# Kernel tuning notes

Measured on AMD Instinct MI355X. Metric: run time of the kernel, lower is better.

The kernel has to match this reference:

```python
import jax, jax.numpy as jnp
import numpy as np

COMMITMENT_COST = 0.25

def setup_inputs() -> dict:
    key = jax.random.key(0)
    k1, k2 = jax.random.split(key)
    z = jax.random.normal(k1, (8, 2048, 768), dtype=jnp.float32)
    # codebook initialized uniform(-1/K, 1/K) in the original; use same scale
    K = 2048
    emb = jax.random.uniform(k2, (K, 768), dtype=jnp.float32, minval=-1.0 / K, maxval=1.0 / K)
    return {"z": z, "emb": emb}

def reference(z, emb):
    B, S, D = z.shape
    z_flat = z.reshape(-1, D)                                   # [N, D]
    # squared-euclidean distances via expansion: ||z||^2 + ||e||^2 - 2 z e^T
    distances = (
        jnp.sum(z_flat * z_flat, axis=1, keepdims=True)
        + jnp.sum(emb * emb, axis=1)
        - 2.0 * jnp.matmul(z_flat, emb.T)
    )                                                           # [N, K]
    ids_flat = jnp.argmin(distances, axis=1)                    # [N]
    z_q = emb[ids_flat].reshape(z.shape)                        # gather + reshape
    concept_ids = ids_flat.reshape(B, S)
    # training path with use_ema=True: codebook_loss = 0, commitment term only.
    # NOTE: original (faithfully) computes mse(z.detach(), z_q) — grad flows to z_q.
    commitment_loss = jnp.mean((jax.lax.stop_gradient(z) - z_q) ** 2)
    vq_loss = COMMITMENT_COST * commitment_loss
    # straight-through estimator
    z_q_st = z + jax.lax.stop_gradient(z_q - z)
    return z_q_st, concept_ids, vq_loss
```

## Files before the change

### kernel.cpp

```cpp
#include <hip/hip_runtime.h>
#include <float.h>

typedef unsigned short ushort_t;
typedef unsigned int uint_t;

#define NROWS 16384
#define DDIM  768
#define KCODES 2048
#define NCB2   8
#define MARGIN 8e-4f

__device__ __forceinline__ ushort_t f2bf(float x) {
    uint_t u = __float_as_uint(x);
    uint_t r = (u + 0x7fffu + ((u >> 16) & 1u)) >> 16;
    return (ushort_t)r;
}
__device__ __forceinline__ float bf2f(ushort_t h) {
    return __uint_as_float(((uint_t)h) << 16);
}

__global__ void prep_kernel(const float* __restrict__ z, const float* __restrict__ emb,
                            float* __restrict__ ee, float* __restrict__ zz,
                            ushort_t* __restrict__ Zh, ushort_t* __restrict__ Eh,
                            float* __restrict__ out_loss) {
    const int b = blockIdx.x, t = threadIdx.x;
    if (b == 0 && t == 0) out_loss[0] = 0.f;
    if (b < KCODES) {
        const int c = b;
        const float* e = emb + (size_t)c * DDIM;
        float s = 0.f;
        for (int i = t; i < DDIM; i += 256) { float v = e[i]; s += v * v; }
        for (int off = 32; off; off >>= 1) s += __shfl_down(s, off);
        __shared__ float red[4];
        if ((t & 63) == 0) red[t >> 6] = s;
        __syncthreads();
        if (t == 0) ee[c] = red[0] + red[1] + red[2] + red[3];
        if (t < 192) {
            const float4 v = ((const float4*)e)[t];
            ushort4 h;
            h.x = f2bf(v.x); h.y = f2bf(v.y); h.z = f2bf(v.z); h.w = f2bf(v.w);
            ((ushort4*)(Eh + (size_t)c * DDIM))[t] = h;
        }
    } else {
        const int rb = b - KCODES;
        const int row = rb * 4 + (t >> 6);
        const int lane = t & 63;
        const float* zr = z + (size_t)row * DDIM;
        float s = 0.f;
        for (int i = lane; i < DDIM; i += 64) { float v = zr[i]; s += v * v; }
        for (int off = 32; off; off >>= 1) s += __shfl_down(s, off);
        if (lane == 0) zz[row] = s;
        const float4* zr4 = (const float4*)zr;
        ushort4* dh = (ushort4*)(Zh + (size_t)row * DDIM);
        #pragma unroll
        for (int j = 0; j < 3; ++j) {
            const int i4 = lane + 64 * j;
            const float4 v = zr4[i4];
            ushort4 h;
            h.x = f2bf(v.x); h.y = f2bf(v.y); h.z = f2bf(v.z); h.w = f2bf(v.w);
            dh[i4] = h;
        }
    }
}

typedef __attribute__((ext_vector_type(8))) short bf16x8;
typedef __attribute__((ext_vector_type(4))) float f32x4;

__device__ __forceinline__ int swz(int r) { return (r & 3) ^ ((r >> 2) & 3); }

__global__ __launch_bounds__(256, 2)
void mfma_kernel(const ushort_t* __restrict__ Ab, const ushort_t* __restrict__ Bb,
                 const float* __restrict__ ee, float* __restrict__ bmin,
                 float2* __restrict__ slots) {
    __shared__ __align__(16) char smem[24576];
    float* rowmin = (float*)smem;
    int*   rcnt   = (int*)(smem + 512);
    float (*sval)[8] = (float(*)[8])(smem + 1024);
    int   (*sidx)[8] = (int(*)[8])(smem + 5120);

    const int t = threadIdx.x;
    const int w = t >> 6, l = t & 63;
    const int bx = blockIdx.x & 127;
    const int by = blockIdx.x >> 7;
    const int row0 = bx << 7;
    const int col0 = by << 8;

    f32x4 acc[4][8];
    #pragma unroll
    for (int i = 0; i < 4; ++i)
        #pragma unroll
        for (int j = 0; j < 8; ++j) acc[i][j] = (f32x4){0.f, 0.f, 0.f, 0.f};

    const int sri = l >> 2, slot = l & 3;
    const ushort_t* gA[2]; uint_t lA[2];
    #pragma unroll
    for (int q = 0; q < 2; ++q) {
        const int r0 = ((w << 1) + q) << 4;
        const int ra = r0 + sri;
        const int c  = slot ^ swz(ra);
        gA[q] = Ab + (size_t)(row0 + ra) * DDIM + (c << 3);
        lA[q] = r0 << 6;
    }
    const ushort_t* gB[4]; uint_t lB[4];
    #pragma unroll
    for (int q = 0; q < 4; ++q) {
        const int r0 = ((w << 2) + q) << 4;
        const int ra = r0 + sri;
        const int c  = slot ^ swz(ra);
        gB[q] = Bb + (size_t)(col0 + ra) * DDIM + (c << 3);
        lB[q] = 8192 + (r0 << 6);
    }

    const int rha = (w & 1) << 6;
    const int chb = (w >> 1) << 7;
    const ushort_t* aAddr[4]; const ushort_t* bAddr[8];
    #pragma unroll
    for (int mi = 0; mi < 4; ++mi) {
        const int r = rha + (mi << 4) + (l & 15);
        const int sw = (l >> 4) ^ swz(r);
        aAddr[mi] = (const ushort_t*)(smem + (r << 6) + (sw << 4));
    }
    #pragma unroll
    for (int ni = 0; ni < 8; ++ni) {
        const int r = chb + (ni << 4) + (l & 15);
        const int sw = (l >> 4) ^ swz(r);
        bAddr[ni] = (const ushort_t*)(smem + 8192 + (r << 6) + (sw << 4));
    }

    for (int kt = 0; kt < 24; ++kt) {
        __syncthreads();
        #pragma unroll
        for (int q = 0; q < 2; ++q) {
            __builtin_amdgcn_global_load_lds(
                (const __attribute__((address_space(1))) void*)gA[q],
                (__attribute__((address_space(3))) void*)(smem + lA[q]), 16, 0, 0);
            gA[q] += 32;
        }
        #pragma unroll
        for (int q = 0; q < 4; ++q) {
            __builtin_amdgcn_global_load_lds(
                (const __attribute__((address_space(1))) void*)gB[q],
                (__attribute__((address_space(3))) void*)(smem + lB[q]), 16, 0, 0);
            gB[q] += 32;
        }
        __syncthreads();

        bf16x8 af[4], bfr[8];
        #pragma unroll
        for (int mi = 0; mi < 4; ++mi) af[mi] = *(const bf16x8*)aAddr[mi];
        #pragma unroll
        for (int ni = 0; ni < 8; ++ni) bfr[ni] = *(const bf16x8*)bAddr[ni];
        #pragma unroll
        for (int mi = 0; mi < 4; ++mi)
            #pragma unroll
            for (int ni = 0; ni < 8; ++ni)
                acc[mi][ni] = __builtin_amdgcn_mfma_f32_16x16x32_bf16(
                    af[mi], bfr[ni], acc[mi][ni], 0, 0, 0);
    }

    __syncthreads();

    float ecv[8];
    #pragma unroll
    for (int ni = 0; ni < 8; ++ni) ecv[ni] = ee[col0 + chb + (ni << 4) + (l & 15)];
    #pragma unroll
    for (int mi = 0; mi < 4; ++mi)
        #pragma unroll
        for (int ni = 0; ni < 8; ++ni)
            #pragma unroll
            for (int r = 0; r < 4; ++r)
                acc[mi][ni][r] = ecv[ni] - 2.0f * acc[mi][ni][r];

    float vmr[4][4];
    #pragma unroll
    for (int mi = 0; mi < 4; ++mi)
        #pragma unroll
        for (int r = 0; r < 4; ++r) {
            float v = acc[mi][0][r];
            #pragma unroll
            for (int ni = 1; ni < 8; ++ni) v = fminf(v, acc[mi][ni][r]);
            v = fminf(v, __shfl_xor(v, 1));
            v = fminf(v, __shfl_xor(v, 2));
            v = fminf(v, __shfl_xor(v, 4));
            v = fminf(v, __shfl_xor(v, 8));
            vmr[mi][r] = v;
        }

    if (t < 128) { rowmin[t] = FLT_MAX; rcnt[t] = 0; }
    __syncthreads();
    if (w < 2 && (l & 15) == 0) {
        #pragma unroll
        for (int mi = 0; mi < 4; ++mi)
            #pragma unroll
            for (int r = 0; r < 4; ++r)
                rowmin[rha + (mi << 4) + ((l >> 4) << 2) + r] = vmr[mi][r];
    }
    __syncthreads();
    if (w >= 2 && (l & 15) == 0) {
        #pragma unroll
        for (int mi = 0; mi < 4; ++mi)
            #pragma unroll
            for (int r = 0; r < 4; ++r) {
                const int m = rha + (mi << 4) + ((l >> 4) << 2) + r;
                rowmin[m] = fminf(rowmin[m], vmr[mi][r]);
            }
    }
    __syncthreads();

    #pragma unroll
    for (int mi = 0; mi < 4; ++mi)
        #pragma unroll
        for (int r = 0; r < 4; ++r) {
            const int m = rha + (mi << 4) + ((l >> 4) << 2) + r;
            const float lim = rowmin[m] + MARGIN;
            #pragma unroll
            for (int ni = 0; ni < 8; ++ni) {
                const float vv = acc[mi][ni][r];
                if (vv <= lim) {
                    const int p = atomicAdd(&rcnt[m], 1);
                    if (p < 8) {
                        sval[m][p] = vv;
                        sidx[m][p] = col0 + chb + (ni << 4) + (l & 15);
                    }
                }
            }
        }
    __syncthreads();

    if (t < 128) {
        const int row = row0 + t;
        bmin[(size_t)by * NROWS + row] = rowmin[t];
        const int n = rcnt[t] < 8 ? rcnt[t] : 8;
        float2 rec[8];
        #pragma unroll
        for (int s2 = 0; s2 < 8; ++s2)
            rec[s2] = (s2 < n) ? make_float2(sval[t][s2], __int_as_float(sidx[t][s2]))
                               : make_float2(FLT_MAX, __int_as_float(0x7fffffff));
        float4* dst = (float4*)(slots + ((size_t)by * NROWS + row) * 8);
        dst[0] = make_float4(rec[0].x, rec[0].y, rec[1].x, rec[1].y);
        dst[1] = make_float4(rec[2].x, rec[2].y, rec[3].x, rec[3].y);
        dst[2] = make_float4(rec[4].x, rec[4].y, rec[5].x, rec[5].y);
        dst[3] = make_float4(rec[6].x, rec[6].y, rec[7].x, rec[7].y);
    }
}

__global__ __launch_bounds__(256)
void combine_select_gather(const float* __restrict__ bmin, const float2* __restrict__ slots,
                           const float* __restrict__ ee, const float* __restrict__ zz,
                           const float* __restrict__ z, const float* __restrict__ emb,
                           float* __restrict__ ids_f32, float* __restrict__ out0,
                           float* __restrict__ out_loss) {
    const int t = threadIdx.x;
    const int w = t >> 6;
    const int row = blockIdx.x * 4 + w;
    const int l = t & 63;

    float v = (l < NCB2) ? bmin[(size_t)l * NROWS + row] : FLT_MAX;
    v = fminf(v, __shfl_xor(v, 4));
    v = fminf(v, __shfl_xor(v, 2));
    v = fminf(v, __shfl_xor(v, 1));
    const float T = __shfl(v, 0) + MARGIN;

    const int blk = l >> 3;
    const int s0 = l & 7;
    const float2 a = slots[((size_t)blk * NROWS + row) * 8 + s0];

    unsigned long long m = __ballot(a.x <= T);

    const float zzr = zz[row];
    const float* zr = z + (size_t)row * DDIM;

    float bestd = FLT_MAX; int besti = 0x7fffffff;
    while (m) {
        const int j = __ffsll(m) - 1; m &= m - 1;
        const int idx = __float_as_int(__shfl(a.y, j));
        const float* er = emb + (size_t)idx * DDIM;
        float p = 0.f;
        #pragma unroll
        for (int k = 0; k < 12; ++k) p += zr[l + 64 * k] * er[l + 64 * k];
        for (int off = 32; off; off >>= 1) p += __shfl_down(p, off);
        if (l == 0) {
            const float t1 = zzr + ee[idx];
            const float d  = t1 - 2.0f * p;
            if (d < bestd || (d == bestd && idx < besti)) { bestd = d; besti = idx; }
        }
    }
    const int bi = __shfl(besti, 0);
    if (l == 0) ids_f32[row] = (float)bi;

    const float4* zr4 = (const float4*)zr;
    const float4* er4 = (const float4*)(emb + (size_t)bi * DDIM);
    float4* o4 = (float4*)(out0 + (size_t)row * DDIM);
    float s = 0.f;
    #pragma unroll
    for (int j = 0; j < 3; ++j) {
        const int i4 = l + 64 * j;
        const float4 zv = zr4[i4];
        const float4 ev = er4[i4];
        float4 o;
        o.x = zv.x + (ev.x - zv.x); o.y = zv.y + (ev.y - zv.y);
        o.z = zv.z + (ev.z - zv.z); o.w = zv.w + (ev.w - zv.w);
        o4[i4] = o;
        const float dx = zv.x - ev.x, dy = zv.y - ev.y;
        const float dz = zv.z - ev.z, dw = zv.w - ev.w;
        s += dx * dx + dy * dy + dz * dz + dw * dw;
    }
    for (int off = 32; off; off >>= 1) s += __shfl_down(s, off);
    __shared__ float lred[4];
    if (l == 0) lred[w] = s;
    __syncthreads();
    if (t == 0) {
        const float tot = lred[0] + lred[1] + lred[2] + lred[3];
        atomicAdd(out_loss, tot * (0.25f / (float)((size_t)NROWS * DDIM)));
    }
}

__global__ void ee_kernel(const float* __restrict__ emb, float* __restrict__ ee) {
    int c = blockIdx.x;
    const float* e = emb + (size_t)c * DDIM;
    int t = threadIdx.x;
    float s = 0.f;
    for (int i = t; i < DDIM; i += 256) { float v = e[i]; s += v * v; }
    for (int off = 32; off; off >>= 1) s += __shfl_down(s, off);
    __shared__ float red[4];
    if ((t & 63) == 0) red[t >> 6] = s;
    __syncthreads();
    if (t == 0) ee[c] = red[0] + red[1] + red[2] + red[3];
}

__global__ void zz_kernel(const float* __restrict__ z, float* __restrict__ zz) {
    const int t = threadIdx.x;
    const int row = blockIdx.x * 4 + (t >> 6);
    const int lane = t & 63;
    const float* zr = z + (size_t)row * DDIM;
    float s = 0.f;
    for (int i = lane; i < DDIM; i += 64) { float v = zr[i]; s += v * v; }
    for (int off = 32; off; off >>= 1) s += __shfl_down(s, off);
    if (lane == 0) zz[row] = s;
}

#define BM 32
#define BN 128
#define BKS 32
#define SPLITC 2
#define CODES_PER_BLOCK (KCODES / SPLITC)
#define NCHUNK (CODES_PER_BLOCK / BN)
#define NSTAGE (DDIM / BKS)
#define APADR 33
#define BPADC 132

__global__ __launch_bounds__(256)
void argmin_kernel(const float* __restrict__ z, const float* __restrict__ emb,
                   const float* __restrict__ ee, const float* __restrict__ zz,
                   float* __restrict__ pval, int* __restrict__ pidx) {
    __shared__ float Af[BKS][APADR];
    __shared__ float Bf[BKS][BPADC];
    __shared__ float cval[BM][33];
    __shared__ int   cidx[BM][33];
    __shared__ float zzs[BM];
    const int t = threadIdx.x;
    const int part = blockIdx.x & (SPLITC - 1);
    const int rb = blockIdx.x >> 1;
    const int row0 = rb * BM;
    const int cbase = part * CODES_PER_BLOCK;
    const int tx = t & 31, ty = t >> 5;
    const int sr = t >> 3;
    const int sk = 4 * (t & 7);
    if (t < BM) zzs[t] = zz[row0 + t];
    float bv[4]; int bi[4];
    #pragma unroll
    for (int i = 0; i < 4; ++i) { bv[i] = FLT_MAX; bi[i] = 0x7fffffff; }
    const float* zt = z + (size_t)(row0 + sr) * DDIM;
    for (int chunk = 0; chunk < NCHUNK; ++chunk) {
        const int c0 = cbase + chunk * BN;
        const float* ebase = emb + (size_t)(c0 + sr) * DDIM;
        float acc[4][4];
        #pragma unroll
        for (int i = 0; i < 4; ++i)
            #pragma unroll
            for (int j = 0; j < 4; ++j) acc[i][j] = 0.f;
        float4 pa = *(const float4*)&zt[sk];
        float4 pb[4];
        #pragma unroll
        for (int m = 0; m < 4; ++m) pb[m] = *(const float4*)&ebase[(size_t)(32 * m) * DDIM + sk];
        for (int s = 0; s < NSTAGE; ++s) {
            __syncthreads();
            Af[sk + 0][sr] = pa.x; Af[sk + 1][sr] = pa.y;
            Af[sk + 2][sr] = pa.z; Af[sk + 3][sr] = pa.w;
            #pragma unroll
            for (int m = 0; m < 4; ++m) {
                Bf[sk + 0][sr + 32 * m] = pb[m].x;
                Bf[sk + 1][sr + 32 * m] = pb[m].y;
                Bf[sk + 2][sr + 32 * m] = pb[m].z;
                Bf[sk + 3][sr + 32 * m] = pb[m].w;
            }
            __syncthreads();
            if (s + 1 < NSTAGE) {
                const int k1 = (s + 1) * BKS + sk;
                pa = *(const float4*)&zt[k1];
                #pragma unroll
                for (int m = 0; m < 4; ++m)
                    pb[m] = *(const float4*)&ebase[(size_t)(32 * m) * DDIM + k1];
            }
            #pragma unroll
            for (int kk = 0; kk < BKS; ++kk) {
                const float4 a4 = *(const float4*)&Af[kk][4 * ty];
                const float4 b4 = *(const float4*)&Bf[kk][4 * tx];
                const float aa[4] = {a4.x, a4.y, a4.z, a4.w};
                const float bb[4] = {b4.x, b4.y, b4.z, b4.w};
                #pragma unroll
                for (int i = 0; i < 4; ++i)
                    #pragma unroll
                    for (int j = 0; j < 4; ++j) acc[i][j] += aa[i] * bb[j];
            }
        }
        const float4 e4 = *(const float4*)&ee[c0 + 4 * tx];
        const float eev[4] = {e4.x, e4.y, e4.z, e4.w};
        #pragma unroll
        for (int i = 0; i < 4; ++i) {
            const float zzr = zzs[4 * ty + i];
            #pragma unroll
            for (int j = 0; j < 4; ++j) {
                const int code = c0 + 4 * tx + j;
                const float t1 = zzr + eev[j];
                const float d  = t1 - 2.0f * acc[i][j];
                if (d < bv[i] || (d == bv[i] && code < bi[i])) { bv[i] = d; bi[i] = code; }
            }
        }
    }
    __syncthreads();
    #pragma unroll
    for (int i = 0; i < 4; ++i) { cval[4 * ty + i][tx] = bv[i]; cidx[4 * ty + i][tx] = bi[i]; }
    __syncthreads();
    if (t < BM) {
        float v = FLT_MAX; int id = 0x7fffffff;
        #pragma unroll
        for (int x = 0; x < 32; ++x) {
            const float cv = cval[t][x]; const int ci = cidx[t][x];
            if (cv < v || (cv == v && ci < id)) { v = cv; id = ci; }
        }
        pval[part * NROWS + row0 + t] = v;
        pidx[part * NROWS + row0 + t] = id;
    }
}

__global__ void combine_kernel(const float* __restrict__ pval, const int* __restrict__ pidx,
                               float* __restrict__ ids_f32) {
    const int r = blockIdx.x * 256 + threadIdx.x;
    float v = pval[r];           int id = pidx[r];
    const float v1 = pval[NROWS + r]; const int i1 = pidx[NROWS + r];
    if (v1 < v || (v1 == v && i1 < id)) { v = v1; id = i1; }
    ids_f32[r] = (float)id;
}

__global__ __launch_bounds__(256)
void gather_kernel(const float* __restrict__ z, const float* __restrict__ emb,
                   const float* __restrict__ ids_f32, float* __restrict__ out0,
                   float* __restrict__ part) {
    const int b = blockIdx.x;
    const int t = threadIdx.x;
    const int rl = t >> 4, c = t & 15;
    __shared__ int ids[16];
    if (t < 16) ids[t] = (int)ids_f32[b * 16 + t];
    __syncthreads();
    const int row = b * 16 + rl;
    const float4* zr = (const float4*)(z + (size_t)row * DDIM);
    float4* orow = (float4*)(out0 + (size_t)row * DDIM);
    const float4* er = (const float4*)(emb + (size_t)ids[rl] * DDIM);
    float s = 0.f;
    #pragma unroll
    for (int j = 0; j < 12; ++j) {
        const int i4 = c + 16 * j;
        const float4 zv = zr[i4];
        const float4 ev = er[i4];
        float4 o;
        o.x = zv.x + (ev.x - zv.x); o.y = zv.y + (ev.y - zv.y);
        o.z = zv.z + (ev.z - zv.z); o.w = zv.w + (ev.w - zv.w);
        orow[i4] = o;
        float dx = zv.x - ev.x, dy = zv.y - ev.y, dz = zv.z - ev.z, dw = zv.w - ev.w;
        s += dx * dx + dy * dy + dz * dz + dw * dw;
    }
    for (int off = 32; off; off >>= 1) s += __shfl_down(s, off);
    __shared__ float red[4];
    if ((t & 63) == 0) red[t >> 6] = s;
    __syncthreads();
    if (t == 0) part[b] = red[0] + red[1] + red[2] + red[3];
}

__global__ void loss_kernel(const float* __restrict__ part, float* __restrict__ out_loss) {
    const int t = threadIdx.x;
    double s = 0.0;
    for (int i = t; i < 1024; i += 256) s += (double)part[i];
    for (int off = 32; off; off >>= 1) s += __shfl_down(s, off);
    __shared__ double red[4];
    if ((t & 63) == 0) red[t >> 6] = s;
    __syncthreads();
    if (t == 0) {
        const double total = red[0] + red[1] + red[2] + red[3];
        out_loss[0] = (float)(0.25 * (total / (double)((size_t)NROWS * DDIM)));
    }
}

#define EE_OFF   0
#define ZZ_OFF   8192
#define EH_OFF   73728
#define ZH_OFF   (EH_OFF + (size_t)KCODES * DDIM * 2)
#define BMIN_OFF (ZH_OFF + (size_t)NROWS * DDIM * 2)
#define SLOT_OFF (BMIN_OFF + (size_t)NCB2 * NROWS * 4)
#define WS_NEED  (SLOT_OFF + (size_t)NCB2 * NROWS * 8 * 8)
#define PART_OFF 73728
#define PV_OFF   81920

extern "C" void kernel_launch(void* const* d_in, const int* in_sizes, int n_in,
                              void* d_out, int out_size, void* d_ws, size_t ws_size,
                              hipStream_t stream) {
    const float* z   = (const float*)d_in[0];
    const float* emb = (const float*)d_in[1];

    float* out0     = (float*)d_out;
    float* out_ids  = out0 + (size_t)NROWS * DDIM;
    float* out_loss = out_ids + NROWS;

    char* ws = (char*)d_ws;
    float* ee   = (float*)(ws + EE_OFF);
    float* zzws = (float*)(ws + ZZ_OFF);

    if (ws_size >= WS_NEED) {
        ushort_t* Eh   = (ushort_t*)(ws + EH_OFF);
        ushort_t* Zh   = (ushort_t*)(ws + ZH_OFF);
        float*    bmin = (float*)(ws + BMIN_OFF);
        float2*   slot = (float2*)(ws + SLOT_OFF);
        prep_kernel<<<KCODES + NROWS / 4, 256, 0, stream>>>(z, emb, ee, zzws, Zh, Eh, out_loss);
        mfma_kernel<<<(NROWS / 128) * NCB2, 256, 0, stream>>>(Zh, Eh, ee, bmin, slot);
        combine_select_gather<<<NROWS / 4, 256, 0, stream>>>(bmin, slot, ee, zzws, z, emb,
                                                             out_ids, out0, out_loss);
    } else {
        float* part = (float*)(ws + PART_OFF);
        float* pval = (float*)(ws + PV_OFF);
        int*   pidx = (int*)(ws + PV_OFF + 131072);
        ee_kernel<<<KCODES, 256, 0, stream>>>(emb, ee);
        zz_kernel<<<NROWS / 4, 256, 0, stream>>>(z, zzws);
        argmin_kernel<<<(NROWS / BM) * SPLITC, 256, 0, stream>>>(z, emb, ee, zzws, pval, pidx);
        combine_kernel<<<NROWS / 256, 256, 0, stream>>>(pval, pidx, out_ids);
        gather_kernel<<<NROWS / 16, 256, 0, stream>>>(z, emb, out_ids, out0, part);
        loss_kernel<<<1, 256, 0, stream>>>(part, out_loss);
    }
}
```

Measured before the change: 241.4 us.

## Fuse bf16 conversion, MFMA distance argmin, refinement and gather into one kernel

The z-to-bf16 conversion, the row-norm computation, the MFMA distance search over all codes, candidate refinement, gather and loss are merged into a single kernel. Each 512-thread block keeps its 64 rows of z in LDS and streams the bf16 codebook through a double-buffered LDS tile in chunks of 128 codes. A running per-row minimum is kept with encoded-float atomicMin, and near-minimum candidates are collected per chunk. This removes the Zh, bmin and slot workspace round trips and two launches. In exchange, each block re-reads the whole codebook, uses small 2x2 MFMA tiles per wave, synchronises every k-step, and the large LDS footprint likely allows only one block per CU.

```diff
diff --git a/kernel.cpp b/kernel.cpp
--- a/kernel.cpp
+++ b/kernel.cpp
@@ -7,7 +7,6 @@
 #define NROWS 16384
 #define DDIM  768
 #define KCODES 2048
-#define NCB2   8
 #define MARGIN 8e-4f
 
 __device__ __forceinline__ ushort_t f2bf(float x) {
@@ -15,302 +14,283 @@
     uint_t r = (u + 0x7fffu + ((u >> 16) & 1u)) >> 16;
     return (ushort_t)r;
 }
-__device__ __forceinline__ float bf2f(ushort_t h) {
-    return __uint_as_float(((uint_t)h) << 16);
-}
-
-__global__ void prep_kernel(const float* __restrict__ z, const float* __restrict__ emb,
-                            float* __restrict__ ee, float* __restrict__ zz,
-                            ushort_t* __restrict__ Zh, ushort_t* __restrict__ Eh,
-                            float* __restrict__ out_loss) {
-    const int b = blockIdx.x, t = threadIdx.x;
-    if (b == 0 && t == 0) out_loss[0] = 0.f;
-    if (b < KCODES) {
-        const int c = b;
-        const float* e = emb + (size_t)c * DDIM;
-        float s = 0.f;
-        for (int i = t; i < DDIM; i += 256) { float v = e[i]; s += v * v; }
-        for (int off = 32; off; off >>= 1) s += __shfl_down(s, off);
-        __shared__ float red[4];
-        if ((t & 63) == 0) red[t >> 6] = s;
-        __syncthreads();
-        if (t == 0) ee[c] = red[0] + red[1] + red[2] + red[3];
-        if (t < 192) {
-            const float4 v = ((const float4*)e)[t];
-            ushort4 h;
-            h.x = f2bf(v.x); h.y = f2bf(v.y); h.z = f2bf(v.z); h.w = f2bf(v.w);
-            ((ushort4*)(Eh + (size_t)c * DDIM))[t] = h;
-        }
-    } else {
-        const int rb = b - KCODES;
-        const int row = rb * 4 + (t >> 6);
-        const int lane = t & 63;
+
+__device__ __forceinline__ uint_t fenc(float f) {
+    uint_t u = __float_as_uint(f);
+    return (u & 0x80000000u) ? ~u : (u | 0x80000000u);
+}
+__device__ __forceinline__ float fdec(uint_t k) {
+    uint_t u = (k & 0x80000000u) ? (k ^ 0x80000000u) : ~k;
+    return __uint_as_float(u);
+}
+
+typedef __attribute__((ext_vector_type(8))) short bf16x8;
+typedef __attribute__((ext_vector_type(4))) float f32x4;
+
+__global__ void prep2_kernel(const float* __restrict__ emb, float* __restrict__ ee,
+                             ushort_t* __restrict__ Eh, float* __restrict__ out_loss) {
+    const int c = blockIdx.x, t = threadIdx.x;
+    if (c == 0 && t == 0) out_loss[0] = 0.f;
+    const float* e = emb + (size_t)c * DDIM;
+    float s = 0.f;
+    for (int i = t; i < DDIM; i += 256) { float v = e[i]; s += v * v; }
+    for (int off = 32; off; off >>= 1) s += __shfl_down(s, off);
+    __shared__ float red[4];
+    if ((t & 63) == 0) red[t >> 6] = s;
+    __syncthreads();
+    if (t == 0) ee[c] = red[0] + red[1] + red[2] + red[3];
+    if (t < 192) {
+        const float4 v = ((const float4*)e)[t];
+        ushort4 h;
+        h.x = f2bf(v.x); h.y = f2bf(v.y); h.z = f2bf(v.z); h.w = f2bf(v.w);
+        ((ushort4*)(Eh + (size_t)c * DDIM))[t] = h;
+    }
+}
+
+#define WGROWS   64
+#define CHUNK    128
+#define NCHUNKS  16
+#define KSTEPS   12
+#define CAP      16
+#define B_OFF    98304
+#define RMIN_OFF 131072
+#define RCNT_OFF 131328
+#define SVAL_OFF 131584
+#define SIDX_OFF 135680
+#define LRED_OFF 139776
+#define SMEM_BYTES 139808
+
+__global__ __launch_bounds__(512, 2)
+void fused_kernel(const float* __restrict__ z, const float* __restrict__ emb,
+                  const ushort_t* __restrict__ Eh, const float* __restrict__ ee,
+                  float* __restrict__ ids_f32, float* __restrict__ out0,
+                  float* __restrict__ out_loss) {
+    __shared__ __align__(16) char smem[SMEM_BYTES];
+    uint_t* rowminU = (uint_t*)(smem + RMIN_OFF);
+    int*    rcnt    = (int*)(smem + RCNT_OFF);
+    float (*sval)[CAP] = (float(*)[CAP])(smem + SVAL_OFF);
+    int   (*sidx)[CAP] = (int(*)[CAP])(smem + SIDX_OFF);
+    float*  lred    = (float*)(smem + LRED_OFF);
+
+    const int t = threadIdx.x;
+    const int w = t >> 6, l = t & 63;
+    const int row0 = blockIdx.x * WGROWS;
+
+    if (t < 64) { rowminU[t] = 0xFFFFFFFFu; rcnt[t] = 0; }
+
+    float zzr[8];
+    #pragma unroll
+    for (int rr = 0; rr < 8; ++rr) {
+        const int row = row0 + w * 8 + rr;
         const float* zr = z + (size_t)row * DDIM;
         float s = 0.f;
-        for (int i = lane; i < DDIM; i += 64) { float v = zr[i]; s += v * v; }
+        #pragma unroll
+        for (int k = 0; k < 12; ++k) { const float v = zr[l + 64 * k]; s += v * v; }
         for (int off = 32; off; off >>= 1) s += __shfl_down(s, off);
-        if (lane == 0) zz[row] = s;
-        const float4* zr4 = (const float4*)zr;
-        ushort4* dh = (ushort4*)(Zh + (size_t)row * DDIM);
-        #pragma unroll
-        for (int j = 0; j < 3; ++j) {
-            const int i4 = lane + 64 * j;
-            const float4 v = zr4[i4];
-            ushort4 h;
-            h.x = f2bf(v.x); h.y = f2bf(v.y); h.z = f2bf(v.z); h.w = f2bf(v.w);
-            dh[i4] = h;
-        }
-    }
-}
-
-typedef __attribute__((ext_vector_type(8))) short bf16x8;
-typedef __attribute__((ext_vector_type(4))) float f32x4;
-
-__device__ __forceinline__ int swz(int r) { return (r & 3) ^ ((r >> 2) & 3); }
-
-__global__ __launch_bounds__(256, 2)
-void mfma_kernel(const ushort_t* __restrict__ Ab, const ushort_t* __restrict__ Bb,
-                 const float* __restrict__ ee, float* __restrict__ bmin,
-                 float2* __restrict__ slots) {
-    __shared__ __align__(16) char smem[24576];
-    float* rowmin = (float*)smem;
-    int*   rcnt   = (int*)(smem + 512);
-    float (*sval)[8] = (float(*)[8])(smem + 1024);
-    int   (*sidx)[8] = (int(*)[8])(smem + 5120);
-
-    const int t = threadIdx.x;
-    const int w = t >> 6, l = t & 63;
-    const int bx = blockIdx.x & 127;
-    const int by = blockIdx.x >> 7;
-    const int row0 = bx << 7;
-    const int col0 = by << 8;
-
-    f32x4 acc[4][8];
-    #pragma unroll
-    for (int i = 0; i < 4; ++i)
-        #pragma unroll
-        for (int j = 0; j < 8; ++j) acc[i][j] = (f32x4){0.f, 0.f, 0.f, 0.f};
-
-    const int sri = l >> 2, slot = l & 3;
-    const ushort_t* gA[2]; uint_t lA[2];
+        zzr[rr] = __shfl(s, 0);
+    }
+
+    {
+        const int ar = t >> 3;
+        const int as = t & 7;
+        const float4* zr4 = (const float4*)(z + (size_t)(row0 + ar) * DDIM);
+        char* abase = smem + ar * 1536;
+        const int rx = (ar & 7) << 4;
+        #pragma unroll
+        for (int j = 0; j < 12; ++j) {
+            const int slot = as + 8 * j;
+            const float4 v0 = zr4[2 * slot];
+            const float4 v1 = zr4[2 * slot + 1];
+            ushort4 h0, h1;
+            h0.x = f2bf(v0.x); h0.y = f2bf(v0.y); h0.z = f2bf(v0.z); h0.w = f2bf(v0.w);
+            h1.x = f2bf(v1.x); h1.y = f2bf(v1.y); h1.z = f2bf(v1.z); h1.w = f2bf(v1.w);
+            char* p = abase + ((slot << 4) ^ rx);
+            *(ushort4*)p = h0;
+            *(ushort4*)(p + 8) = h1;
+        }
+    }
+
+    const int brow_l  = l >> 3;
+    const int srcslot = (l & 7) ^ brow_l;
+    const ushort_t* gB[2];
     #pragma unroll
     for (int q = 0; q < 2; ++q) {
-        const int r0 = ((w << 1) + q) << 4;
-        const int ra = r0 + sri;
-        const int c  = slot ^ swz(ra);
-        gA[q] = Ab + (size_t)(row0 + ra) * DDIM + (c << 3);
-        lA[q] = r0 << 6;
-    }
-    const ushort_t* gB[4]; uint_t lB[4];
-    #pragma unroll
-    for (int q = 0; q < 4; ++q) {
-        const int r0 = ((w << 2) + q) << 4;
-        const int ra = r0 + sri;
-        const int c  = slot ^ swz(ra);
-        gB[q] = Bb + (size_t)(col0 + ra) * DDIM + (c << 3);
-        lB[q] = 8192 + (r0 << 6);
-    }
-
-    const int rha = (w & 1) << 6;
-    const int chb = (w >> 1) << 7;
-    const ushort_t* aAddr[4]; const ushort_t* bAddr[8];
-    #pragma unroll
-    for (int mi = 0; mi < 4; ++mi) {
-        const int r = rha + (mi << 4) + (l & 15);
-        const int sw = (l >> 4) ^ swz(r);
-        aAddr[mi] = (const ushort_t*)(smem + (r << 6) + (sw << 4));
-    }
-    #pragma unroll
-    for (int ni = 0; ni < 8; ++ni) {
-        const int r = chb + (ni << 4) + (l & 15);
-        const int sw = (l >> 4) ^ swz(r);
-        bAddr[ni] = (const ushort_t*)(smem + 8192 + (r << 6) + (sw << 4));
-    }
-
-    for (int kt = 0; kt < 24; ++kt) {
+        const int grow = q * 64 + w * 8 + brow_l;
+        gB[q] = Eh + (size_t)grow * DDIM + srcslot * 8;
+    }
+
+    const int wr = w >> 2, wc = w & 3;
+    const int g = l >> 4, lr = l & 15;
+    int aoff[2][2], boff[2][2];
+    #pragma unroll
+    for (int mi = 0; mi < 2; ++mi) {
+        const int arow = wr * 32 + mi * 16 + lr;
+        #pragma unroll
+        for (int kf = 0; kf < 2; ++kf)
+            aoff[mi][kf] = arow * 1536 + ((((kf << 2) + g) << 4) ^ ((arow & 7) << 4));
+    }
+    #pragma unroll
+    for (int ni = 0; ni < 2; ++ni) {
+        const int brow = wc * 32 + ni * 16 + lr;
+        #pragma unroll
+        for (int kf = 0; kf < 2; ++kf)
+            boff[ni][kf] = brow * 128 + ((((kf << 2) + g) << 4) ^ ((brow & 7) << 4));
+    }
+
+    int cur = 0;
+    #pragma unroll
+    for (int q = 0; q < 2; ++q) {
+        __builtin_amdgcn_global_load_lds(
+            (const __attribute__((address_space(1))) void*)gB[q],
+            (__attribute__((address_space(3))) void*)(smem + B_OFF + q * 8192 + w * 1024),
+            16, 0, 0);
+        gB[q] += 64;
+    }
+    __syncthreads();
+
+    for (int c = 0; c < NCHUNKS; ++c) {
+        const int c0 = c * CHUNK;
+        f32x4 acc[2][2];
+        #pragma unroll
+        for (int mi = 0; mi < 2; ++mi)
+            #pragma unroll
+            for (int ni = 0; ni < 2; ++ni) acc[mi][ni] = (f32x4){0.f, 0.f, 0.f, 0.f};
+
+        for (int s = 0; s < KSTEPS; ++s) {
+            if (!(c == NCHUNKS - 1 && s == KSTEPS - 1)) {
+                const int nb = B_OFF + (cur ^ 1) * 16384 + w * 1024;
+                #pragma unroll
+                for (int q = 0; q < 2; ++q)
+                    __builtin_amdgcn_global_load_lds(
+                        (const __attribute__((address_space(1))) void*)gB[q],
+                        (__attribute__((address_space(3))) void*)(smem + nb + q * 8192),
+                        16, 0, 0);
+                const int adv = (s == KSTEPS - 2) ? (64 + 127 * 768) : 64;
+                gB[0] += adv; gB[1] += adv;
+            }
+            const char* Bb = smem + B_OFF + cur * 16384;
+            bf16x8 af[2][2], bfv[2][2];
+            #pragma unroll
+            for (int mi = 0; mi < 2; ++mi)
+                #pragma unroll
+                for (int kf = 0; kf < 2; ++kf)
+                    af[mi][kf] = *(const bf16x8*)(smem + aoff[mi][kf] + s * 128);
+            #pragma unroll
+            for (int ni = 0; ni < 2; ++ni)
+                #pragma unroll
+                for (int kf = 0; kf < 2; ++kf)
+                    bfv[ni][kf] = *(const bf16x8*)(Bb + boff[ni][kf]);
+            #pragma unroll
+            for (int kf = 0; kf < 2; ++kf)
+                #pragma unroll
+                for (int mi = 0; mi < 2; ++mi)
+                    #pragma unroll
+                    for (int ni = 0; ni < 2; ++ni)
+                        acc[mi][ni] = __builtin_amdgcn_mfma_f32_16x16x32_bf16(
+                            af[mi][kf], bfv[ni][kf], acc[mi][ni], 0, 0, 0);
+            __syncthreads();
+            cur ^= 1;
+        }
+
+        float ecv[2];
+        #pragma unroll
+        for (int ni = 0; ni < 2; ++ni) ecv[ni] = ee[c0 + wc * 32 + ni * 16 + lr];
+        float dv[2][2][4];
+        #pragma unroll
+        for (int mi = 0; mi < 2; ++mi)
+            #pragma unroll
+            for (int ni = 0; ni < 2; ++ni)
+                #pragma unroll
+                for (int r = 0; r < 4; ++r)
+                    dv[mi][ni][r] = ecv[ni] - 2.0f * acc[mi][ni][r];
+
+        #pragma unroll
+        for (int mi = 0; mi < 2; ++mi)
+            #pragma unroll
+            for (int r = 0; r < 4; ++r) {
+                float v = fminf(dv[mi][0][r], dv[mi][1][r]);
+                v = fminf(v, __shfl_xor(v, 1));
+                v = fminf(v, __shfl_xor(v, 2));
+                v = fminf(v, __shfl_xor(v, 4));
+                v = fminf(v, __shfl_xor(v, 8));
+                if (lr == 0) atomicMin(&rowminU[wr * 32 + mi * 16 + g * 4 + r], fenc(v));
+            }
         __syncthreads();
         #pragma unroll
-        for (int q = 0; q < 2; ++q) {
-            __builtin_amdgcn_global_load_lds(
-                (const __attribute__((address_space(1))) void*)gA[q],
-                (__attribute__((address_space(3))) void*)(smem + lA[q]), 16, 0, 0);
-            gA[q] += 32;
-        }
-        #pragma unroll
-        for (int q = 0; q < 4; ++q) {
-            __builtin_amdgcn_global_load_lds(
-                (const __attribute__((address_space(1))) void*)gB[q],
-                (__attribute__((address_space(3))) void*)(smem + lB[q]), 16, 0, 0);
-            gB[q] += 32;
-        }
-        __syncthreads();
-
-        bf16x8 af[4], bfr[8];
-        #pragma unroll
-        for (int mi = 0; mi < 4; ++mi) af[mi] = *(const bf16x8*)aAddr[mi];
-        #pragma unroll
-        for (int ni = 0; ni < 8; ++ni) bfr[ni] = *(const bf16x8*)bAddr[ni];
-        #pragma unroll
-        for (int mi = 0; mi < 4; ++mi)
-            #pragma unroll
-            for (int ni = 0; ni < 8; ++ni)
-                acc[mi][ni] = __builtin_amdgcn_mfma_f32_16x16x32_bf16(
-                    af[mi], bfr[ni], acc[mi][ni], 0, 0, 0);
-    }
-
-    __syncthreads();
-
-    float ecv[8];
-    #pragma unroll
-    for (int ni = 0; ni < 8; ++ni) ecv[ni] = ee[col0 + chb + (ni << 4) + (l & 15)];
-    #pragma unroll
-    for (int mi = 0; mi < 4; ++mi)
-        #pragma unroll
-        for (int ni = 0; ni < 8; ++ni)
-            #pragma unroll
-            for (int r = 0; r < 4; ++r)
-                acc[mi][ni][r] = ecv[ni] - 2.0f * acc[mi][ni][r];
-
-    float vmr[4][4];
-    #pragma unroll
-    for (int mi = 0; mi < 4; ++mi)
-        #pragma unroll
-        for (int r = 0; r < 4; ++r) {
-            float v = acc[mi][0][r];
-            #pragma unroll
-            for (int ni = 1; ni < 8; ++ni) v = fminf(v, acc[mi][ni][r]);
-            v = fminf(v, __shfl_xor(v, 1));
-            v = fminf(v, __shfl_xor(v, 2));
-            v = fminf(v, __shfl_xor(v, 4));
-            v = fminf(v, __shfl_xor(v, 8));
-            vmr[mi][r] = v;
-        }
-
-    if (t < 128) { rowmin[t] = FLT_MAX; rcnt[t] = 0; }
-    __syncthreads();
-    if (w < 2 && (l & 15) == 0) {
-        #pragma unroll
-        for (int mi = 0; mi < 4; ++mi)
-            #pragma unroll
-            for (int r = 0; r < 4; ++r)
-                rowmin[rha + (mi << 4) + ((l >> 4) << 2) + r] = vmr[mi][r];
-    }
-    __syncthreads();
-    if (w >= 2 && (l & 15) == 0) {
-        #pragma unroll
-        for (int mi = 0; mi < 4; ++mi)
+        for (int mi = 0; mi < 2; ++mi)
             #pragma unroll
             for (int r = 0; r < 4; ++r) {
-                const int m = rha + (mi << 4) + ((l >> 4) << 2) + r;
-                rowmin[m] = fminf(rowmin[m], vmr[mi][r]);
-            }
-    }
-    __syncthreads();
-
-    #pragma unroll
-    for (int mi = 0; mi < 4; ++mi)
-        #pragma unroll
-        for (int r = 0; r < 4; ++r) {
-            const int m = rha + (mi << 4) + ((l >> 4) << 2) + r;
-            const float lim = rowmin[m] + MARGIN;
-            #pragma unroll
-            for (int ni = 0; ni < 8; ++ni) {
-                const float vv = acc[mi][ni][r];
-                if (vv <= lim) {
-                    const int p = atomicAdd(&rcnt[m], 1);
-                    if (p < 8) {
-                        sval[m][p] = vv;
-                        sidx[m][p] = col0 + chb + (ni << 4) + (l & 15);
+                const int lrow = wr * 32 + mi * 16 + g * 4 + r;
+                const float lim = fdec(rowminU[lrow]) + MARGIN;
+                #pragma unroll
+                for (int ni = 0; ni < 2; ++ni) {
+                    const float vv = dv[mi][ni][r];
+                    if (vv <= lim) {
+                        const int p = atomicAdd(&rcnt[lrow], 1);
+                        if (p < CAP) {
+                            sval[lrow][p] = vv;
+                            sidx[lrow][p] = c0 + wc * 32 + ni * 16 + lr;
+                        }
                     }
                 }
             }
-        }
-    __syncthreads();
-
-    if (t < 128) {
-        const int row = row0 + t;
-        bmin[(size_t)by * NROWS + row] = rowmin[t];
-        const int n = rcnt[t] < 8 ? rcnt[t] : 8;
-        float2 rec[8];
-        #pragma unroll
-        for (int s2 = 0; s2 < 8; ++s2)
-            rec[s2] = (s2 < n) ? make_float2(sval[t][s2], __int_as_float(sidx[t][s2]))
-                               : make_float2(FLT_MAX, __int_as_float(0x7fffffff));
-        float4* dst = (float4*)(slots + ((size_t)by * NROWS + row) * 8);
-        dst[0] = make_float4(rec[0].x, rec[0].y, rec[1].x, rec[1].y);
-        dst[1] = make_float4(rec[2].x, rec[2].y, rec[3].x, rec[3].y);
-        dst[2] = make_float4(rec[4].x, rec[4].y, rec[5].x, rec[5].y);
-        dst[3] = make_float4(rec[6].x, rec[6].y, rec[7].x, rec[7].y);
-    }
-}
-
-__global__ __launch_bounds__(256)
-void combine_select_gather(const float* __restrict__ bmin, const float2* __restrict__ slots,
-                           const float* __restrict__ ee, const float* __restrict__ zz,
-                           const float* __restrict__ z, const float* __restrict__ emb,
-                           float* __restrict__ ids_f32, float* __restrict__ out0,
-                           float* __restrict__ out_loss) {
-    const int t = threadIdx.x;
-    const int w = t >> 6;
-    const int row = blockIdx.x * 4 + w;
-    const int l = t & 63;
-
-    float v = (l < NCB2) ? bmin[(size_t)l * NROWS + row] : FLT_MAX;
-    v = fminf(v, __shfl_xor(v, 4));
-    v = fminf(v, __shfl_xor(v, 2));
-    v = fminf(v, __shfl_xor(v, 1));
-    const float T = __shfl(v, 0) + MARGIN;
-
-    const int blk = l >> 3;
-    const int s0 = l & 7;
-    const float2 a = slots[((size_t)blk * NROWS + row) * 8 + s0];
-
-    unsigned long long m = __ballot(a.x <= T);
-
-    const float zzr = zz[row];
-    const float* zr = z + (size_t)row * DDIM;
-
-    float bestd = FLT_MAX; int besti = 0x7fffffff;
-    while (m) {
-        const int j = __ffsll(m) - 1; m &= m - 1;
-        const int idx = __float_as_int(__shfl(a.y, j));
-        const float* er = emb + (size_t)idx * DDIM;
-        float p = 0.f;
-        #pragma unroll
-        for (int k = 0; k < 12; ++k) p += zr[l + 64 * k] * er[l + 64 * k];
-        for (int off = 32; off; off >>= 1) p += __shfl_down(p, off);
-        if (l == 0) {
-            const float t1 = zzr + ee[idx];
-            const float d  = t1 - 2.0f * p;
-            if (d < bestd || (d == bestd && idx < besti)) { bestd = d; besti = idx; }
-        }
-    }
-    const int bi = __shfl(besti, 0);
-    if (l == 0) ids_f32[row] = (float)bi;
-
-    const float4* zr4 = (const float4*)zr;
-    const float4* er4 = (const float4*)(emb + (size_t)bi * DDIM);
-    float4* o4 = (float4*)(out0 + (size_t)row * DDIM);
-    float s = 0.f;
-    #pragma unroll
-    for (int j = 0; j < 3; ++j) {
-        const int i4 = l + 64 * j;
-        const float4 zv = zr4[i4];
-        const float4 ev = er4[i4];
-        float4 o;
-        o.x = zv.x + (ev.x - zv.x); o.y = zv.y + (ev.y - zv.y);
-        o.z = zv.z + (ev.z - zv.z); o.w = zv.w + (ev.w - zv.w);
-        o4[i4] = o;
-        const float dx = zv.x - ev.x, dy = zv.y - ev.y;
-        const float dz = zv.z - ev.z, dw = zv.w - ev.w;
-        s += dx * dx + dy * dy + dz * dz + dw * dw;
-    }
-    for (int off = 32; off; off >>= 1) s += __shfl_down(s, off);
-    __shared__ float lred[4];
-    if (l == 0) lred[w] = s;
+    }
+    __syncthreads();
+
+    float wloss = 0.f;
+    for (int rr = 0; rr < 8; ++rr) {
+        const int lrow = w * 8 + rr;
+        const int row = row0 + lrow;
+        const float T = fdec(rowminU[lrow]) + MARGIN;
+        const int n = rcnt[lrow] < CAP ? rcnt[lrow] : CAP;
+        float val = FLT_MAX; int idx = 0x7fffffff;
+        if (l < n) { val = sval[lrow][l]; idx = sidx[lrow][l]; }
+        unsigned long long m = __ballot(val <= T);
+        const float* zr = z + (size_t)row * DDIM;
+        float bestd = FLT_MAX; int besti = 0x7fffffff;
+        while (m) {
+            const int j = __ffsll(m) - 1; m &= m - 1;
+            const int cand = __shfl(idx, j);
+            const float* er = emb + (size_t)cand * DDIM;
+            float p = 0.f;
+            #pragma unroll
+            for (int k = 0; k < 12; ++k) p += zr[l + 64 * k] * er[l + 64 * k];
+            for (int off = 32; off; off >>= 1) p += __shfl_down(p, off);
+            if (l == 0) {
+                const float t1 = zzr[rr] + ee[cand];
+                const float d  = t1 - 2.0f * p;
+                if (d < bestd || (d == bestd && cand < besti)) { bestd = d; besti = cand; }
+            }
+        }
+        const int bi = __shfl(besti, 0);
+        if (l == 0) ids_f32[row] = (float)bi;
+
+        const float4* zr4 = (const float4*)zr;
+        const float4* er4 = (const float4*)(emb + (size_t)bi * DDIM);
+        float4* o4 = (float4*)(out0 + (size_t)row * DDIM);
+        float s = 0.f;
+        #pragma unroll
+        for (int j2 = 0; j2 < 3; ++j2) {
+            const int i4 = l + 64 * j2;
+            const float4 zv = zr4[i4];
+            const float4 ev = er4[i4];
+            float4 o;
+            o.x = zv.x + (ev.x - zv.x); o.y = zv.y + (ev.y - zv.y);
+            o.z = zv.z + (ev.z - zv.z); o.w = zv.w + (ev.w - zv.w);
+            o4[i4] = o;
+            const float dx = zv.x - ev.x, dy = zv.y - ev.y;
+            const float dz = zv.z - ev.z, dw = zv.w - ev.w;
+            s += dx * dx + dy * dy + dz * dz + dw * dw;
+        }
+        for (int off = 32; off; off >>= 1) s += __shfl_down(s, off);
+        if (l == 0) wloss += s;
+    }
+    if (l == 0) lred[w] = wloss;
     __syncthreads();
     if (t == 0) {
-        const float tot = lred[0] + lred[1] + lred[2] + lred[3];
+        float tot = 0.f;
+        #pragma unroll
+        for (int i = 0; i < 8; ++i) tot += lred[i];
         atomicAdd(out_loss, tot * (0.25f / (float)((size_t)NROWS * DDIM)));
     }
 }
@@ -504,10 +484,7 @@
 #define EE_OFF   0
 #define ZZ_OFF   8192
 #define EH_OFF   73728
-#define ZH_OFF   (EH_OFF + (size_t)KCODES * DDIM * 2)
-#define BMIN_OFF (ZH_OFF + (size_t)NROWS * DDIM * 2)
-#define SLOT_OFF (BMIN_OFF + (size_t)NCB2 * NROWS * 4)
-#define WS_NEED  (SLOT_OFF + (size_t)NCB2 * NROWS * 8 * 8)
+#define WS_NEED  (EH_OFF + (size_t)KCODES * DDIM * 2)
 #define PART_OFF 73728
 #define PV_OFF   81920
 
@@ -526,14 +503,10 @@
     float* zzws = (float*)(ws + ZZ_OFF);
 
     if (ws_size >= WS_NEED) {
-        ushort_t* Eh   = (ushort_t*)(ws + EH_OFF);
-        ushort_t* Zh   = (ushort_t*)(ws + ZH_OFF);
-        float*    bmin = (float*)(ws + BMIN_OFF);
-        float2*   slot = (float2*)(ws + SLOT_OFF);
-        prep_kernel<<<KCODES + NROWS / 4, 256, 0, stream>>>(z, emb, ee, zzws, Zh, Eh, out_loss);
-        mfma_kernel<<<(NROWS / 128) * NCB2, 256, 0, stream>>>(Zh, Eh, ee, bmin, slot);
-        combine_select_gather<<<NROWS / 4, 256, 0, stream>>>(bmin, slot, ee, zzws, z, emb,
-                                                             out_ids, out0, out_loss);
+        ushort_t* Eh = (ushort_t*)(ws + EH_OFF);
+        prep2_kernel<<<KCODES, 256, 0, stream>>>(emb, ee, Eh, out_loss);
+        fused_kernel<<<NROWS / WGROWS, 512, 0, stream>>>(z, emb, Eh, ee,
+                                                         out_ids, out0, out_loss);
     } else {
         float* part = (float*)(ws + PART_OFF);
         float* pval = (float*)(ws + PV_OFF);
```

Measured after the change: 250.9 us. 3.9% more time.

## Triple-buffer MFMA K-loop with async LDS ring and single-candidate fast path

Applied to the files above, without the earlier changes.

Replaces the single-buffer load/sync/compute loop with a three-stage LDS ring. Global-to-LDS loads for the tile two steps ahead are issued before the MFMAs on the current tile, and completion is tracked with vmcnt waits and one barrier per iteration instead of two. The row-min reduction becomes a shared-memory atomicMin on order-preserving encoded floats. The combine kernel also skips the exact fp32 re-check when only one candidate survives. LDS use grows threefold, which may limit occupancy. Skipping the re-check trusts the bf16 candidate when it is the only one within the margin.

```diff
diff --git a/kernel.cpp b/kernel.cpp
--- a/kernel.cpp
+++ b/kernel.cpp
@@ -15,8 +15,14 @@
     uint_t r = (u + 0x7fffu + ((u >> 16) & 1u)) >> 16;
     return (ushort_t)r;
 }
-__device__ __forceinline__ float bf2f(ushort_t h) {
-    return __uint_as_float(((uint_t)h) << 16);
+
+__device__ __forceinline__ uint_t fenc(float f) {
+    uint_t u = __float_as_uint(f);
+    return (u & 0x80000000u) ? ~u : (u | 0x80000000u);
+}
+__device__ __forceinline__ float fdec(uint_t k) {
+    uint_t u = (k & 0x80000000u) ? (k ^ 0x80000000u) : ~k;
+    return __uint_as_float(u);
 }
 
 __global__ void prep_kernel(const float* __restrict__ z, const float* __restrict__ emb,
@@ -68,15 +74,18 @@
 
 __device__ __forceinline__ int swz(int r) { return (r & 3) ^ ((r >> 2) & 3); }
 
+#define RINGB 24576
+#define CAPS  8
+
 __global__ __launch_bounds__(256, 2)
-void mfma_kernel(const ushort_t* __restrict__ Ab, const ushort_t* __restrict__ Bb,
-                 const float* __restrict__ ee, float* __restrict__ bmin,
-                 float2* __restrict__ slots) {
-    __shared__ __align__(16) char smem[24576];
-    float* rowmin = (float*)smem;
-    int*   rcnt   = (int*)(smem + 512);
-    float (*sval)[8] = (float(*)[8])(smem + 1024);
-    int   (*sidx)[8] = (int(*)[8])(smem + 5120);
+void mfma_ring_kernel(const ushort_t* __restrict__ Ab, const ushort_t* __restrict__ Bb,
+                      const float* __restrict__ ee, float* __restrict__ bmin,
+                      float2* __restrict__ slots) {
+    __shared__ __align__(16) char smem[3 * RINGB];
+    uint_t* rowminU = (uint_t*)smem;
+    int*    rcnt    = (int*)(smem + 512);
+    float (*sval)[CAPS] = (float(*)[CAPS])(smem + 1024);
+    int   (*sidx)[CAPS] = (int(*)[CAPS])(smem + 5120);
 
     const int t = threadIdx.x;
     const int w = t >> 6, l = t & 63;
@@ -113,51 +122,77 @@
 
     const int rha = (w & 1) << 6;
     const int chb = (w >> 1) << 7;
-    const ushort_t* aAddr[4]; const ushort_t* bAddr[8];
+    int aoff[4], boff[8];
     #pragma unroll
     for (int mi = 0; mi < 4; ++mi) {
         const int r = rha + (mi << 4) + (l & 15);
         const int sw = (l >> 4) ^ swz(r);
-        aAddr[mi] = (const ushort_t*)(smem + (r << 6) + (sw << 4));
+        aoff[mi] = (r << 6) + (sw << 4);
     }
     #pragma unroll
     for (int ni = 0; ni < 8; ++ni) {
         const int r = chb + (ni << 4) + (l & 15);
         const int sw = (l >> 4) ^ swz(r);
-        bAddr[ni] = (const ushort_t*)(smem + 8192 + (r << 6) + (sw << 4));
-    }
-
+        boff[ni] = 8192 + (r << 6) + (sw << 4);
+    }
+
+#define STAGE(base_) do {                                                     \
+        _Pragma("unroll")                                                     \
+        for (int q = 0; q < 2; ++q) {                                         \
+            __builtin_amdgcn_global_load_lds(                                 \
+                (const __attribute__((address_space(1))) void*)gA[q],         \
+                (__attribute__((address_space(3))) void*)(smem + (base_) + lA[q]), \
+                16, 0, 0);                                                    \
+            gA[q] += 32;                                                      \
+        }                                                                     \
+        _Pragma("unroll")                                                     \
+        for (int q = 0; q < 4; ++q) {                                         \
+            __builtin_amdgcn_global_load_lds(                                 \
+                (const __attribute__((address_space(1))) void*)gB[q],         \
+                (__attribute__((address_space(3))) void*)(smem + (base_) + lB[q]), \
+                16, 0, 0);                                                    \
+            gB[q] += 32;                                                      \
+        }                                                                     \
+    } while (0)
+
+    STAGE(0);
+    STAGE(RINGB);
+    __syncthreads();
+
+    int cur = 0, stg = 2;
     for (int kt = 0; kt < 24; ++kt) {
-        __syncthreads();
-        #pragma unroll
-        for (int q = 0; q < 2; ++q) {
-            __builtin_amdgcn_global_load_lds(
-                (const __attribute__((address_space(1))) void*)gA[q],
-                (__attribute__((address_space(3))) void*)(smem + lA[q]), 16, 0, 0);
-            gA[q] += 32;
-        }
-        #pragma unroll
-        for (int q = 0; q < 4; ++q) {
-            __builtin_amdgcn_global_load_lds(
-                (const __attribute__((address_space(1))) void*)gB[q],
-                (__attribute__((address_space(3))) void*)(smem + lB[q]), 16, 0, 0);
-            gB[q] += 32;
-        }
-        __syncthreads();
-
+        if (kt < 22) STAGE((uint_t)stg * RINGB);
+
+        const char* cb_ = smem + (uint_t)cur * RINGB;
         bf16x8 af[4], bfr[8];
         #pragma unroll
-        for (int mi = 0; mi < 4; ++mi) af[mi] = *(const bf16x8*)aAddr[mi];
-        #pragma unroll
-        for (int ni = 0; ni < 8; ++ni) bfr[ni] = *(const bf16x8*)bAddr[ni];
+        for (int mi = 0; mi < 4; ++mi) af[mi] = *(const bf16x8*)(cb_ + aoff[mi]);
+        #pragma unroll
+        for (int ni = 0; ni < 8; ++ni) bfr[ni] = *(const bf16x8*)(cb_ + boff[ni]);
+
+        __builtin_amdgcn_s_setprio(1);
         #pragma unroll
         for (int mi = 0; mi < 4; ++mi)
             #pragma unroll
             for (int ni = 0; ni < 8; ++ni)
                 acc[mi][ni] = __builtin_amdgcn_mfma_f32_16x16x32_bf16(
                     af[mi], bfr[ni], acc[mi][ni], 0, 0, 0);
-    }
-
+        __builtin_amdgcn_s_setprio(0);
+
+        if (kt < 22) asm volatile("s_waitcnt vmcnt(6)" ::: "memory");
+        else         asm volatile("s_waitcnt vmcnt(0)" ::: "memory");
+        __builtin_amdgcn_sched_barrier(0);
+        __builtin_amdgcn_s_barrier();
+        __builtin_amdgcn_sched_barrier(0);
+
+        cur = (cur == 2) ? 0 : cur + 1;
+        stg = (stg == 2) ? 0 : stg + 1;
+    }
+#undef STAGE
+
+    __syncthreads();
+
+    if (t < 128) { rowminU[t] = 0xFFFFFFFFu; rcnt[t] = 0; }
     __syncthreads();
 
     float ecv[8];
@@ -171,7 +206,6 @@
             for (int r = 0; r < 4; ++r)
                 acc[mi][ni][r] = ecv[ni] - 2.0f * acc[mi][ni][r];
 
-    float vmr[4][4];
     #pragma unroll
     for (int mi = 0; mi < 4; ++mi)
         #pragma unroll
@@ -183,28 +217,9 @@
             v = fminf(v, __shfl_xor(v, 2));
             v = fminf(v, __shfl_xor(v, 4));
             v = fminf(v, __shfl_xor(v, 8));
-            vmr[mi][r] = v;
-        }
-
-    if (t < 128) { rowmin[t] = FLT_MAX; rcnt[t] = 0; }
-    __syncthreads();
-    if (w < 2 && (l & 15) == 0) {
-        #pragma unroll
-        for (int mi = 0; mi < 4; ++mi)
-            #pragma unroll
-            for (int r = 0; r < 4; ++r)
-                rowmin[rha + (mi << 4) + ((l >> 4) << 2) + r] = vmr[mi][r];
-    }
-    __syncthreads();
-    if (w >= 2 && (l & 15) == 0) {
-        #pragma unroll
-        for (int mi = 0; mi < 4; ++mi)
-            #pragma unroll
-            for (int r = 0; r < 4; ++r) {
-                const int m = rha + (mi << 4) + ((l >> 4) << 2) + r;
-                rowmin[m] = fminf(rowmin[m], vmr[mi][r]);
-            }
-    }
+            if ((l & 15) == 0)
+                atomicMin(&rowminU[rha + (mi << 4) + ((l >> 4) << 2) + r], fenc(v));
+        }
     __syncthreads();
 
     #pragma unroll
@@ -212,13 +227,13 @@
         #pragma unroll
         for (int r = 0; r < 4; ++r) {
             const int m = rha + (mi << 4) + ((l >> 4) << 2) + r;
-            const float lim = rowmin[m] + MARGIN;
+            const float lim = fdec(rowminU[m]) + MARGIN;
             #pragma unroll
             for (int ni = 0; ni < 8; ++ni) {
                 const float vv = acc[mi][ni][r];
                 if (vv <= lim) {
                     const int p = atomicAdd(&rcnt[m], 1);
-                    if (p < 8) {
+                    if (p < CAPS) {
                         sval[m][p] = vv;
                         sidx[m][p] = col0 + chb + (ni << 4) + (l & 15);
                     }
@@ -229,8 +244,8 @@
 
     if (t < 128) {
         const int row = row0 + t;
-        bmin[(size_t)by * NROWS + row] = rowmin[t];
-        const int n = rcnt[t] < 8 ? rcnt[t] : 8;
+        bmin[(size_t)by * NROWS + row] = fdec(rowminU[t]);
+        const int n = rcnt[t] < CAPS ? rcnt[t] : CAPS;
         float2 rec[8];
         #pragma unroll
         for (int s2 = 0; s2 < 8; ++s2)
@@ -267,25 +282,29 @@
 
     unsigned long long m = __ballot(a.x <= T);
 
-    const float zzr = zz[row];
     const float* zr = z + (size_t)row * DDIM;
-
-    float bestd = FLT_MAX; int besti = 0x7fffffff;
-    while (m) {
-        const int j = __ffsll(m) - 1; m &= m - 1;
-        const int idx = __float_as_int(__shfl(a.y, j));
-        const float* er = emb + (size_t)idx * DDIM;
-        float p = 0.f;
-        #pragma unroll
-        for (int k = 0; k < 12; ++k) p += zr[l + 64 * k] * er[l + 64 * k];
-        for (int off = 32; off; off >>= 1) p += __shfl_down(p, off);
-        if (l == 0) {
-            const float t1 = zzr + ee[idx];
-            const float d  = t1 - 2.0f * p;
-            if (d < bestd || (d == bestd && idx < besti)) { bestd = d; besti = idx; }
-        }
-    }
-    const int bi = __shfl(besti, 0);
+    int bi;
+    if (__popcll(m) == 1) {
+        bi = __float_as_int(__shfl(a.y, __ffsll(m) - 1));
+    } else {
+        const float zzr = zz[row];
+        float bestd = FLT_MAX; int besti = 0x7fffffff;
+        while (m) {
+            const int j = __ffsll(m) - 1; m &= m - 1;
+            const int idx = __float_as_int(__shfl(a.y, j));
+            const float* er = emb + (size_t)idx * DDIM;
+            float p = 0.f;
+            #pragma unroll
+            for (int k = 0; k < 12; ++k) p += zr[l + 64 * k] * er[l + 64 * k];
+            for (int off = 32; off; off >>= 1) p += __shfl_down(p, off);
+            if (l == 0) {
+                const float t1 = zzr + ee[idx];
+                const float d  = t1 - 2.0f * p;
+                if (d < bestd || (d == bestd && idx < besti)) { bestd = d; besti = idx; }
+            }
+        }
+        bi = __shfl(besti, 0);
+    }
     if (l == 0) ids_f32[row] = (float)bi;
 
     const float4* zr4 = (const float4*)zr;
@@ -531,7 +550,7 @@
         float*    bmin = (float*)(ws + BMIN_OFF);
         float2*   slot = (float2*)(ws + SLOT_OFF);
         prep_kernel<<<KCODES + NROWS / 4, 256, 0, stream>>>(z, emb, ee, zzws, Zh, Eh, out_loss);
-        mfma_kernel<<<(NROWS / 128) * NCB2, 256, 0, stream>>>(Zh, Eh, ee, bmin, slot);
+        mfma_ring_kernel<<<(NROWS / 128) * NCB2, 256, 0, stream>>>(Zh, Eh, ee, bmin, slot);
         combine_select_gather<<<NROWS / 4, 256, 0, stream>>>(bmin, slot, ee, zzws, z, emb,
                                                              out_ids, out0, out_loss);
     } else {
```

Result: no change. 242.0 us (+0.2%).
